# Kernel optimization log

Hardware: AMD Instinct MI355X
Metric: run time of the kernel (lower is better)

## Reference

```python
import jax, jax.numpy as jnp
import numpy as np
from jax import lax

B, N, S, P, FIN, FFUT, H, NB, TOPK = 4, 1437, 56, 28, 10, 6, 64, 2, 5


def layer_norm(x, g, b, eps=1e-5):
    m = x.mean(-1, keepdims=True)
    v = ((x - m) ** 2).mean(-1, keepdims=True)
    return (x - m) * lax.rsqrt(v + eps) * g + b


def conv1d_same(x, w, pl, pr):
    # x: [BNF, 1, S], w: [1, 1, k]; torch Conv1d is cross-correlation == XLA conv
    return lax.conv_general_dilated(x, w, (1,), [(pl, pr)], dimension_numbers=('NCH', 'OIH', 'NCH'))


def gelu(x):
    return jax.nn.gelu(x, approximate=False)


def mixer_block(x, adj, wk, mk, lcg, lcb, ltg, ltb, lfg, lfb, lsg, lsb, tw, tb, fw, fb, sw, sb):
    Bx, Nx, Sx, Fx = x.shape
    # conv branch (pre-norm)
    xn = layer_norm(x, lcg, lcb)
    xc = xn.transpose(0, 1, 3, 2).reshape(Bx * Nx * Fx, 1, Sx)
    weekly = conv1d_same(xc, wk, 3, 3).reshape(Bx, Nx, Fx, Sx).transpose(0, 1, 3, 2)
    monthly = conv1d_same(xc, mk, 13, 14).reshape(Bx, Nx, Fx, Sx).transpose(0, 1, 3, 2)
    x = x + weekly + monthly
    # temporal MLP over S
    xn = layer_norm(x, ltg, ltb)
    xt = gelu(jnp.einsum('bnfs,os->bnfo', xn.transpose(0, 1, 3, 2), tw) + tb)
    x = x + xt.transpose(0, 1, 3, 2)
    # feature MLP over Feat
    xn = layer_norm(x, lfg, lfb)
    x = x + gelu(jnp.einsum('bnsf,of->bnso', xn, fw) + fb)
    # spatial propagation via dense bmm with adj
    xn = layer_norm(x, lsg, lsb)
    xp = jnp.einsum('bnsf,of->bnso', xn, sw).reshape(Bx, Nx, Sx * Fx)
    xs = jnp.einsum('bmn,bnd->bmd', adj, xp).reshape(Bx, Nx, Sx, Fx) + sb
    return x + xs


def reference(x, x_future, adj, fp_w, fp_b, in_ln_g, in_ln_b, q_w, q_b, k_w, k_b,
              node_emb, graph_alpha, blk_weekly, blk_monthly,
              blk_lnc_g, blk_lnc_b, blk_lnt_g, blk_lnt_b, blk_lnf_g, blk_lnf_b,
              blk_lns_g, blk_lns_b, blk_temp_w, blk_temp_b, blk_feat_w, blk_feat_b,
              blk_spat_w, blk_spat_b, futr_w, futr_b, head_w, head_b):
    Bx, Nx, Sx, _ = x.shape
    h = jnp.einsum('bnsf,hf->bnsh', x, fp_w) + fp_b
    h = layer_norm(h, in_ln_g, in_ln_b)
    emb = node_emb / jnp.maximum(jnp.linalg.norm(node_emb, axis=-1, keepdims=True), 1e-12)
    h = h + emb[None, :, None, :]
    # recency-weighted context
    decay = jnp.exp(-jnp.arange(Sx, 0, -1, dtype=jnp.float32) / 14.0)
    rw = decay / decay.sum()
    ctx = (h * rw[None, None, :, None]).sum(2)  # [B,N,H]
    Q = ctx @ q_w.T + q_b
    K = ctx @ k_w.T + k_b
    da = jnp.einsum('bnh,bmh->bnm', Q, K) / jnp.sqrt(jnp.float32(Q.shape[-1]))
    da = jax.nn.relu(jnp.clip(da, -10.0, 10.0))
    _, ti = lax.top_k(da, TOPK)
    mask = jax.vmap(jax.vmap(lambda row, idx: row.at[idx].set(1.0)))(
        jnp.zeros((Bx, Nx, Nx), da.dtype), ti)
    dyn = jax.nn.softmax(jnp.where(mask > 0, da, -jnp.inf), axis=2)
    dyn = jnp.nan_to_num(dyn)
    alpha = jax.nn.sigmoid(graph_alpha)  # shape (1,), broadcasts
    comb = alpha * adj[None, :, :] + (1.0 - alpha) * dyn
    comb = comb / jnp.maximum(jnp.abs(comb).sum(axis=2, keepdims=True), 1e-12)
    for i in range(NB):
        h = mixer_block(h, comb, blk_weekly[i], blk_monthly[i],
                        blk_lnc_g[i], blk_lnc_b[i], blk_lnt_g[i], blk_lnt_b[i],
                        blk_lnf_g[i], blk_lnf_b[i], blk_lns_g[i], blk_lns_b[i],
                        blk_temp_w[i], blk_temp_b[i], blk_feat_w[i], blk_feat_b[i],
                        blk_spat_w[i], blk_spat_b[i])
    hist = h.reshape(Bx, Nx, -1)
    fut = (jnp.einsum('bnpf,hf->bnph', x_future, futr_w) + futr_b).reshape(Bx, Nx, -1)
    feats = jnp.concatenate([hist, fut], axis=2)
    return feats @ head_w.T + head_b


def setup_inputs() -> dict:
    key = jax.random.key(0)
    ks = jax.random.split(key, 16)
    rn = lambda k, shp, s=1.0: jax.random.normal(k, shp, dtype=jnp.float32) * s
    return {
        'x': rn(ks[0], (B, N, S, FIN)),
        'x_future': rn(ks[1], (B, N, P, FFUT)),
        'adj': jax.random.uniform(ks[2], (N, N), dtype=jnp.float32),
        'fp_w': rn(ks[3], (H, FIN), 0.1), 'fp_b': jnp.zeros((H,), jnp.float32),
        'in_ln_g': jnp.ones((H,), jnp.float32), 'in_ln_b': jnp.zeros((H,), jnp.float32),
        'q_w': rn(ks[4], (H, H), 0.1), 'q_b': jnp.zeros((H,), jnp.float32),
        'k_w': rn(ks[5], (H, H), 0.1), 'k_b': jnp.zeros((H,), jnp.float32),
        'node_emb': rn(ks[6], (N, H), 0.02),
        'graph_alpha': jnp.full((1,), 2.2, jnp.float32),
        'blk_weekly': rn(ks[7], (NB, 1, 1, 7), 0.1),
        'blk_monthly': rn(ks[8], (NB, 1, 1, 28), 0.1),
        'blk_lnc_g': jnp.ones((NB, H), jnp.float32), 'blk_lnc_b': jnp.zeros((NB, H), jnp.float32),
        'blk_lnt_g': jnp.ones((NB, H), jnp.float32), 'blk_lnt_b': jnp.zeros((NB, H), jnp.float32),
        'blk_lnf_g': jnp.ones((NB, H), jnp.float32), 'blk_lnf_b': jnp.zeros((NB, H), jnp.float32),
        'blk_lns_g': jnp.ones((NB, H), jnp.float32), 'blk_lns_b': jnp.zeros((NB, H), jnp.float32),
        'blk_temp_w': rn(ks[9], (NB, S, S), 0.1), 'blk_temp_b': jnp.zeros((NB, S), jnp.float32),
        'blk_feat_w': rn(ks[10], (NB, H, H), 0.1), 'blk_feat_b': jnp.zeros((NB, H), jnp.float32),
        'blk_spat_w': rn(ks[11], (NB, H, H), 0.1), 'blk_spat_b': jnp.zeros((NB, H), jnp.float32),
        'futr_w': rn(ks[12], (H, FFUT), 0.1), 'futr_b': jnp.zeros((H,), jnp.float32),
        'head_w': rn(ks[13], (P, S * H + P * H), 0.02), 'head_b': jnp.zeros((P,), jnp.float32),
    }
```

## Files before the change

### kernel.cpp

```cpp
#include <hip/hip_runtime.h>
#include <hip/hip_bf16.h>
#include <math.h>

#define BB 4
#define NN 1437
#define SS 56
#define PP 28
#define FIN 10
#define FFUT 6
#define HH 64
#define NBLK 2
#define TOPK 5
#define DD (SS*HH)
#define FD (PP*HH)
#define TOT (DD+FD)
#define MP 1536
#define KP 1472
#define KC8 (KP/8)
#define NT (KP/32)
#define WIMG_SZ 16384

typedef __attribute__((ext_vector_type(8))) __bf16 bf16x8;
typedef __attribute__((ext_vector_type(4))) float  f32x4;
typedef unsigned long long u64;


__device__ __forceinline__ float gelu_fast(float x){
    float x2 = x*x;
    float u  = __builtin_fmaf(0.044715f*x2, x, x);
    float e  = __builtin_amdgcn_exp2f(2.3022077f*u);
    float r  = __builtin_amdgcn_rcpf(e+1.f);
    return x - x*r;
}
template<int C>
__device__ __forceinline__ float dppadd(float v){
    int x = __builtin_amdgcn_mov_dpp(__float_as_int(v), C, 0xF, 0xF, true);
    return v + __int_as_float(x);
}
__device__ __forceinline__ float row16_sum(float v){
    v = dppadd<0xB1>(v);
    v = dppadd<0x4E>(v);
    v = dppadd<0x141>(v);
    v = dppadd<0x140>(v);
    return v;
}
__device__ __forceinline__ float wave_sum64(float v){
    v = row16_sum(v);
    v += __shfl_xor(v,16,64);
    v += __shfl_xor(v,32,64);
    return v;
}
__device__ __forceinline__ void async_load16(const void* g, void* l){
    __builtin_amdgcn_global_load_lds(
        (const __attribute__((address_space(1))) void*)g,
        (__attribute__((address_space(3))) void*)l, 16, 0, 0);
}
__device__ __forceinline__ unsigned short f2bf(float x){
    unsigned int u = __float_as_uint(x);
    unsigned int r = (u + 0x7fffu + ((u>>16)&1u)) >> 16;
    return (unsigned short)r;
}
__device__ __forceinline__ unsigned int cvtpk_bf16(float lo, float hi){
    unsigned int r;
    asm("v_cvt_pk_bf16_f32 %0, %1, %2" : "=v"(r) : "v"(lo), "v"(hi));
    return r;
}
__device__ __forceinline__ float bf2f(unsigned short u){
    return __uint_as_float(((unsigned int)u)<<16);
}
__device__ __forceinline__ unsigned char f2fp8(float x){
    return (unsigned char)(__builtin_amdgcn_cvt_pk_fp8_f32(x, 0.f, 0, false) & 0xFF);
}
__device__ __forceinline__ unsigned int pack4fp8(float a, float b, float c, float d){
    int lo = __builtin_amdgcn_cvt_pk_fp8_f32(a, b, 0, false);
    return (unsigned int)__builtin_amdgcn_cvt_pk_fp8_f32(c, d, lo, true);
}
__device__ __forceinline__ u64 umax64(u64 a, u64 b){return a>b?a:b;}
__device__ __forceinline__ u64 umin64(u64 a, u64 b){return a<b?a:b;}

#define INS5(a0,a1,a2,a3,a4,x) do{ u64 t_=(x); \
    u64 n0_=umax64(a0,t_), t1_=umin64(a0,t_); \
    u64 n1_=umax64(a1,t1_), t2_=umin64(a1,t1_); \
    u64 n2_=umax64(a2,t2_), t3_=umin64(a2,t2_); \
    u64 n3_=umax64(a3,t3_), t4_=umin64(a3,t3_); \
    u64 n4_=umax64(a4,t4_); \
    a0=n0_;a1=n1_;a2=n2_;a3=n3_;a4=n4_; }while(0)

#define MERGE5(a0,a1,a2,a3,a4,b0,b1,b2,b3,b4) do{ \
    u64 o0_=umax64(a0,(b0)); \
    u64 o1_=umax64(umax64((b1),umin64(a0,(b0))),a1); \
    u64 o2_=umax64(umax64((b2),umin64(a0,(b1))),umax64(umin64(a1,(b0)),a2)); \
    u64 o3_=umax64(umax64((b3),umin64(a0,(b2))),umax64(umin64(a1,(b1)),umax64(umin64(a2,(b0)),a3))); \
    u64 o4_=umax64(umax64((b4),umin64(a0,(b3))),umax64(umax64(umin64(a1,(b2)),umin64(a2,(b1))),umax64(umin64(a3,(b0)),a4))); \
    a0=o0_;a1=o1_;a2=o2_;a3=o3_;a4=o4_; }while(0)

__global__ __launch_bounds__(256) void k_front(
    const float* __restrict__ x, const float* __restrict__ fpw, const float* __restrict__ fpb,
    const float* __restrict__ lng, const float* __restrict__ lnb,
    const float* __restrict__ nemb,
    const float* __restrict__ qw, const float* __restrict__ qb,
    const float* __restrict__ kw, const float* __restrict__ kb,
    float* __restrict__ h,
    unsigned short* __restrict__ qpack, unsigned short* __restrict__ kpack)
{
    int bn = blockIdx.x; int n = bn % NN;
    int tid=threadIdx.x; int lane=tid&63; int wv=tid>>6;
    __shared__ float xin[SS*FIN];
    __shared__ float wlds[HH*FIN];
    __shared__ float rw[SS];
    __shared__ float rsum;
    __shared__ float red[4][HH];
    __shared__ float ctxs[HH];
    for (int i=tid;i<SS*FIN;i+=256) xin[i]=x[(size_t)bn*SS*FIN+i];
    for (int i=tid;i<HH*FIN;i+=256) wlds[i]=fpw[i];
    if (tid<SS) rw[tid]=expf(-(float)(SS-tid)/14.0f);
    __syncthreads();
    if (tid==0){ float s=0.f; for(int i=0;i<SS;++i) s+=rw[i]; rsum=s; }
    __syncthreads();
    float inv_rs = 1.0f/rsum;
    float ev = nemb[(size_t)n*HH+lane];
    float ss = wave_sum64(ev*ev);
    float el = ev / fmaxf(sqrtf(ss), 1e-12f);
    float gg=lng[lane], bv=lnb[lane], fb0=fpb[lane];
    int paddr = (lane&15)*4 + (lane>>4);
    float cacc=0.f;
    for (int s=wv;s<SS;s+=4){
        float v=fb0;
        #pragma unroll
        for (int c=0;c<FIN;++c) v += xin[s*FIN+c]*wlds[lane*FIN+c];
        float m = wave_sum64(v)*(1.f/HH);
        float d = v-m;
        float va = wave_sum64(d*d)*(1.f/HH);
        float hn = d*rsqrtf(va+1e-5f)*gg + bv + el;
        h[((size_t)bn*SS+s)*HH + paddr]=hn;
        cacc += hn * rw[s]*inv_rs;
    }
    red[wv][lane]=cacc;
    __syncthreads();
    if (wv==0) ctxs[lane]=red[0][lane]+red[1][lane]+red[2][lane]+red[3][lane];
    __syncthreads();
    if (wv==0){
        const float4* qr = reinterpret_cast<const float4*>(qw + (size_t)lane*HH);
        const float4* kr = reinterpret_cast<const float4*>(kw + (size_t)lane*HH);
        float q=qb[lane], k=kb[lane];
        #pragma unroll 4
        for (int t=0;t<16;++t){
            float4 qv=qr[t], kv=kr[t];
            float c0=ctxs[4*t], c1=ctxs[4*t+1], c2=ctxs[4*t+2], c3=ctxs[4*t+3];
            q += qv.x*c0+qv.y*c1+qv.z*c2+qv.w*c3;
            k += kv.x*c0+kv.y*c1+kv.z*c2+kv.w*c3;
        }
        int b = bn/NN, m = bn%NN;
        size_t off = (size_t)b*8*MP*8 + (size_t)(lane>>3)*MP*8 + (size_t)m*8 + (lane&7);
        qpack[off]=f2bf(q); kpack[off]=f2bf(k);
    }
}

__global__ __launch_bounds__(256) void k_adjsum(
    const float* __restrict__ adj, float* __restrict__ adjsum)
{
    int m = blockIdx.x*4 + (threadIdx.x>>6);
    int lane = threadIdx.x & 63;
    if (m >= NN) return;
    const float* row = adj + (size_t)m*NN;
    float s=0.f;
    for (int n=lane;n<NN;n+=64) s += row[n];
    s = wave_sum64(s);
    if (lane==0) adjsum[m]=s;
}

__global__ __launch_bounds__(256) void k_qkt_top5(
    const unsigned short* __restrict__ qp, const unsigned short* __restrict__ kp,
    const float* __restrict__ adjsum, const float* __restrict__ galpha,
    int* __restrict__ meta_idx, float* __restrict__ meta_p, float* __restrict__ meta_inv)
{
    int m0 = blockIdx.x*32; int b = blockIdx.y;
    int tid=threadIdx.x, lane=tid&63, w=tid>>6;
    int g=lane>>4, c15=lane&15;
    int wr=w>>1, wc=w&1;
    __shared__ u64 mls[64][5];

    const unsigned short* qb2 = qp + (size_t)b*8*MP*8;
    const unsigned short* kb2 = kp + (size_t)b*8*MP*8;
    bf16x8 af0 = *(const bf16x8*)(qb2 + ((size_t)(0*4+g)*MP + m0+wr*16+c15)*8);
    bf16x8 af1 = *(const bf16x8*)(qb2 + ((size_t)(1*4+g)*MP + m0+wr*16+c15)*8);

    u64 A0=0,A1=0,A2=0,A3=0,A4=0;
    u64 B0=0,B1=0,B2=0,B3=0,B4=0;
    u64 C0=0,C1=0,C2=0,C3=0,C4=0;
    u64 D0=0,D1=0,D2=0,D3=0,D4=0;

    for (int t=0;t<12;++t){
        int n0 = t*128;
        f32x4 acc[4];
        #pragma unroll
        for (int j=0;j<4;++j) acc[j]=(f32x4){0.f,0.f,0.f,0.f};
        #pragma unroll
        for (int j=0;j<4;++j){
            bf16x8 b0 = *(const bf16x8*)(kb2 + ((size_t)(0*4+g)*MP + n0+wc*64+j*16+c15)*8);
            bf16x8 b1 = *(const bf16x8*)(kb2 + ((size_t)(1*4+g)*MP + n0+wc*64+j*16+c15)*8);
            acc[j]=__builtin_amdgcn_mfma_f32_16x16x32_bf16(af0,b0,acc[j],0,0,0);
            acc[j]=__builtin_amdgcn_mfma_f32_16x16x32_bf16(af1,b1,acc[j],0,0,0);
        }
        #pragma unroll
        for (int j=0;j<4;++j){
            int n = n0 + wc*64 + j*16 + c15;
            bool ok = (n < NN);
            unsigned int lowk = 0xFFFFFFFFu - (unsigned)n;
            #define MKKEY(Q) ({ \
                float v_ = acc[j][Q]*0.125f; \
                v_ = fminf(fmaxf(v_,0.f),10.f); \
                ok ? (((u64)__float_as_uint(v_)<<32)|(u64)lowk) : 0ULL; })
            { u64 k_=MKKEY(0); INS5(A0,A1,A2,A3,A4,k_); }
            { u64 k_=MKKEY(1); INS5(B0,B1,B2,B3,B4,k_); }
            { u64 k_=MKKEY(2); INS5(C0,C1,C2,C3,C4,k_); }
            { u64 k_=MKKEY(3); INS5(D0,D1,D2,D3,D4,k_); }
            #undef MKKEY
        }
    }
    #pragma unroll
    for (int off=1; off<16; off<<=1){
        u64 t0,t1,t2,t3,t4;
        t0=__shfl_xor(A0,off,64); t1=__shfl_xor(A1,off,64); t2=__shfl_xor(A2,off,64); t3=__shfl_xor(A3,off,64); t4=__shfl_xor(A4,off,64);
        MERGE5(A0,A1,A2,A3,A4,t0,t1,t2,t3,t4);
        t0=__shfl_xor(B0,off,64); t1=__shfl_xor(B1,off,64); t2=__shfl_xor(B2,off,64); t3=__shfl_xor(B3,off,64); t4=__shfl_xor(B4,off,64);
        MERGE5(B0,B1,B2,B3,B4,t0,t1,t2,t3,t4);
        t0=__shfl_xor(C0,off,64); t1=__shfl_xor(C1,off,64); t2=__shfl_xor(C2,off,64); t3=__shfl_xor(C3,off,64); t4=__shfl_xor(C4,off,64);
        MERGE5(C0,C1,C2,C3,C4,t0,t1,t2,t3,t4);
        t0=__shfl_xor(D0,off,64); t1=__shfl_xor(D1,off,64); t2=__shfl_xor(D2,off,64); t3=__shfl_xor(D3,off,64); t4=__shfl_xor(D4,off,64);
        MERGE5(D0,D1,D2,D3,D4,t0,t1,t2,t3,t4);
    }
    if (c15==0){
        int rb = wr*16 + g*4;
        mls[(rb+0)*2+wc][0]=A0; mls[(rb+0)*2+wc][1]=A1; mls[(rb+0)*2+wc][2]=A2; mls[(rb+0)*2+wc][3]=A3; mls[(rb+0)*2+wc][4]=A4;
        mls[(rb+1)*2+wc][0]=B0; mls[(rb+1)*2+wc][1]=B1; mls[(rb+1)*2+wc][2]=B2; mls[(rb+1)*2+wc][3]=B3; mls[(rb+1)*2+wc][4]=B4;
        mls[(rb+2)*2+wc][0]=C0; mls[(rb+2)*2+wc][1]=C1; mls[(rb+2)*2+wc][2]=C2; mls[(rb+2)*2+wc][3]=C3; mls[(rb+2)*2+wc][4]=C4;
        mls[(rb+3)*2+wc][0]=D0; mls[(rb+3)*2+wc][1]=D1; mls[(rb+3)*2+wc][2]=D2; mls[(rb+3)*2+wc][3]=D3; mls[(rb+3)*2+wc][4]=D4;
    }
    __syncthreads();
    if (tid < 32){
        int m = m0 + tid;
        if (m < NN){
            u64 u0=mls[tid*2][0],u1=mls[tid*2][1],u2=mls[tid*2][2],u3=mls[tid*2][3],u4=mls[tid*2][4];
            MERGE5(u0,u1,u2,u3,u4, mls[tid*2+1][0],mls[tid*2+1][1],mls[tid*2+1][2],mls[tid*2+1][3],mls[tid*2+1][4]);
            float s0=__uint_as_float((unsigned)(u0>>32)), s1=__uint_as_float((unsigned)(u1>>32)),
                  s2=__uint_as_float((unsigned)(u2>>32)), s3=__uint_as_float((unsigned)(u3>>32)),
                  s4=__uint_as_float((unsigned)(u4>>32));
            int i0=(int)(0xFFFFFFFFu-(unsigned)u0), i1=(int)(0xFFFFFFFFu-(unsigned)u1),
                i2=(int)(0xFFFFFFFFu-(unsigned)u2), i3=(int)(0xFFFFFFFFu-(unsigned)u3),
                i4=(int)(0xFFFFFFFFu-(unsigned)u4);
            float e0=1.f, e1=expf(s1-s0), e2=expf(s2-s0), e3=expf(s3-s0), e4=expf(s4-s0);
            float den=e0+e1+e2+e3+e4;
            float alpha=1.f/(1.f+expf(-galpha[0]));
            float oma=(1.f-alpha)/den;
            size_t base = ((size_t)b*NN + m)*5;
            meta_idx[base+0]=i0; meta_idx[base+1]=i1; meta_idx[base+2]=i2; meta_idx[base+3]=i3; meta_idx[base+4]=i4;
            meta_p[base+0]=oma*e0; meta_p[base+1]=oma*e1; meta_p[base+2]=oma*e2; meta_p[base+3]=oma*e3; meta_p[base+4]=oma*e4;
            meta_inv[(size_t)b*NN+m] = 1.f/fmaxf(alpha*adjsum[m] + (1.f-alpha), 1e-12f);
        }
    }
}

__global__ __launch_bounds__(256) void k_blend(
    const float* __restrict__ adj, const float* __restrict__ galpha,
    const int* __restrict__ meta_idx, const float* __restrict__ meta_p,
    unsigned char* __restrict__ comb8)
{
    int bid = blockIdx.x;
    int xx = bid & 7, ii = bid >> 3;
    int lin = (xx < 4) ? xx*719 + ii : 2876 + (xx-4)*718 + ii;
    int b = lin / NN, m = lin - b*NN;
    int tid=threadIdx.x;
    size_t base = ((size_t)b*NN + m)*5;
    int i0=meta_idx[base+0], i1=meta_idx[base+1], i2=meta_idx[base+2],
        i3=meta_idx[base+3], i4=meta_idx[base+4];
    float p0=meta_p[base+0], p1=meta_p[base+1], p2=meta_p[base+2],
          p3=meta_p[base+3], p4=meta_p[base+4];
    float alpha=1.f/(1.f+expf(-galpha[0]));
    const float* arow = adj + (size_t)m*NN;
    unsigned char* dst = comb8 + (size_t)b*KC8*(size_t)MP*8;
    for (int n4=tid; n4<KP/4; n4+=256){
        float v[4];
        #pragma unroll
        for (int k=0;k<4;++k){
            int n = n4*4+k;
            float vv = 0.f;
            if (n<NN){
                vv = alpha*arow[n];
                vv += (n==i0)?p0:0.f;
                vv += (n==i1)?p1:0.f;
                vv += (n==i2)?p2:0.f;
                vv += (n==i3)?p3:0.f;
                vv += (n==i4)?p4:0.f;
            }
            v[k]=vv;
        }
        int kc = n4>>1, half = n4&1;
        *reinterpret_cast<unsigned int*>(dst + ((size_t)kc*MP + m)*8 + half*4) =
            pack4fp8(v[0],v[1],v[2],v[3]);
    }
}

__global__ __launch_bounds__(256) void k_prepw(
    const float* __restrict__ wk, const float* __restrict__ mk,
    const float* __restrict__ tw, const float* __restrict__ fw,
    const float* __restrict__ sw, unsigned short* __restrict__ wimg)
{
    int i = blockIdx.x; int tid = threadIdx.x;
    const float* wki = wk + i*7;
    const float* mki = mk + i*28;
    const float* twi = tw + i*SS*SS;
    const float* fwi = fw + i*HH*HH;
    const float* swi = sw + i*HH*HH;
    unsigned short* o = wimg + (size_t)i*WIMG_SZ;
    for (int e=tid; e<4096; e+=256){
        int r = e>>6, k = e&63;
        int swz = ((k*2) ^ ((r&7)<<4)) >> 1;
        float mv = 0.f;
        if (r<SS && k<SS){
            int a = k-r+3;  if (a>=0 && a<7)  mv += wki[a];
            int b2= k-r+13; if (b2>=0 && b2<28) mv += mki[b2];
        }
        o[r*64 + swz] = f2bf(mv);
        float tv = (r<SS && k<SS) ? twi[r*SS+k] : 0.f;
        o[4096 + r*64 + swz] = f2bf(tv);
        int pk = (k>>3)*512 + r*8 + (k&7);
        o[8192  + pk] = f2bf(fwi[r*HH+k]);
        o[12288 + pk] = f2bf(swi[r*HH+k]);
    }
}

__global__ __launch_bounds__(256) void k_prep_head(
    const float* __restrict__ hw, __hip_bfloat16* __restrict__ hw16)
{
    int i = blockIdx.x*256 + threadIdx.x;
    int r = i / TOT, k = i - r*TOT;
    float v = (r<PP) ? hw[(size_t)r*TOT + k] : 0.f;
    hw16[i] = __float2bfloat16(v);
}

__global__ __launch_bounds__(256) void k_fut(
    const float* __restrict__ xf, const float* __restrict__ fw,
    const float* __restrict__ fbias, __hip_bfloat16* __restrict__ feats)
{
    int bn=blockIdx.x, tid=threadIdx.x;
    __shared__ float fwl[HH*FFUT];
    __shared__ float fbl[HH];
    __shared__ float xfl[PP*FFUT];
    for (int i=tid;i<HH*FFUT;i+=256) fwl[i]=fw[i];
    if (tid<HH) fbl[tid]=fbias[tid];
    for (int i=tid;i<PP*FFUT;i+=256) xfl[i]=xf[(size_t)bn*PP*FFUT+i];
    __syncthreads();
    __hip_bfloat16* dst = feats + (size_t)bn*TOT + DD;
    for (int q=tid;q<FD;q+=256){
        int pp=q>>6, hh2=q&63;
        float v=fbl[hh2];
        #pragma unroll
        for (int c2=0;c2<FFUT;++c2) v += xfl[pp*FFUT+c2]*fwl[hh2*FFUT+c2];
        dst[q]=__float2bfloat16(v);
    }
}

__global__ __launch_bounds__(256) void k_mixer2(
    float* __restrict__ h, unsigned char* __restrict__ xpg8,
    const unsigned short* __restrict__ spat_in,
    const unsigned short* __restrict__ wimg,
    const float* __restrict__ lncg, const float* __restrict__ lncb,
    const float* __restrict__ lntg, const float* __restrict__ lntb,
    const float* __restrict__ lnfg, const float* __restrict__ lnfb,
    const float* __restrict__ lnsg, const float* __restrict__ lnsb,
    const float* __restrict__ tb, const float* __restrict__ fb)
{
    int bid = blockIdx.x;
    int xx = bid & 7, ii = bid >> 3;
    int bn = (xx < 4) ? xx*719 + ii : 2876 + (xx-4)*718 + ii;
    int tid=threadIdx.x, lane=tid&63, w=tid>>6;
    int g=lane>>4, c=lane&15;
    __shared__ unsigned short wbuf[2][4096];
    __shared__ unsigned short xsA[4096];
    __shared__ unsigned short xsB[4096];
    __shared__ float prm[640];

    const char* wsrc=(const char*)wimg;
#define LOADW(SLOTB, BUFP) do{ \
    async_load16(wsrc+(size_t)(SLOTB)+((size_t)tid)*16,       (char*)(BUFP)+(w*64)*16); \
    async_load16(wsrc+(size_t)(SLOTB)+((size_t)(256+tid))*16, (char*)(BUFP)+((256+w*64))*16); } while(0)

    LOADW(0,    wbuf[0]);
    LOADW(8192, wbuf[1]);
    if (tid<64){
        prm[tid]      =lncg[tid]; prm[64+tid] =lncb[tid];
        prm[128+tid]  =lntg[tid]; prm[192+tid]=lntb[tid];
        prm[256+tid]  =lnfg[tid]; prm[320+tid]=lnfb[tid];
        prm[384+tid]  =lnsg[tid]; prm[448+tid]=lnsb[tid];
        prm[512+tid]  =(tid<SS)?tb[tid]:0.f;
        prm[576+tid]  =fb[tid];
    }
    float xl[4][4];
    float* hb = h + (size_t)bn*DD;
    int srow = 16*w + 4*g;
    #pragma unroll
    for (int q=0;q<4;++q){
        int s=srow+q;
        if (s<SS){
            const float4 v4 = *reinterpret_cast<const float4*>(hb + s*HH + c*4);
            float a0=v4.x, a1=v4.y, a2=v4.z, a3=v4.w;
            if (spat_in){
                ushort4 sv = *reinterpret_cast<const ushort4*>(spat_in + (size_t)bn*TOT + s*HH + c*4);
                a0 += bf2f(sv.x); a1 += bf2f(sv.y); a2 += bf2f(sv.z); a3 += bf2f(sv.w);
            }
            xl[q][0]=a0; xl[q][1]=a1; xl[q][2]=a2; xl[q][3]=a3;
        } else {
            xl[q][0]=0.f; xl[q][1]=0.f; xl[q][2]=0.f; xl[q][3]=0.f;
        }
    }
    __syncthreads();

    float xn[4][4];
    f32x4 acc[4];

#define LNSTAGE(GOFF,BOFF) do{ \
    _Pragma("unroll") \
    for (int q=0;q<4;++q){ \
        float sv = xl[q][0]+xl[q][1]+xl[q][2]+xl[q][3]; \
        float s2 = xl[q][0]*xl[q][0]+xl[q][1]*xl[q][1]+xl[q][2]*xl[q][2]+xl[q][3]*xl[q][3]; \
        sv = row16_sum(sv); \
        s2 = row16_sum(s2); \
        float mn = sv*(1.f/64.f); \
        float var = s2*(1.f/64.f)-mn*mn; \
        float rstd = rsqrtf(var+1e-5f); \
        bool ok = (srow+q)<SS; \
        _Pragma("unroll") \
        for (int tj=0;tj<4;++tj){ \
            float v=(xl[q][tj]-mn)*rstd*prm[(GOFF)+tj*16+c]+prm[(BOFF)+tj*16+c]; \
            xn[q][tj]= ok ? v : 0.f; \
        } \
    } }while(0)

#define WRITE_XNP(XS) do{ \
    _Pragma("unroll") \
    for (int qp=0;qp<2;++qp){ \
        int s0=srow+2*qp; \
        _Pragma("unroll") \
        for (int tj=0;tj<4;++tj){ \
            unsigned int pv = cvtpk_bf16(xn[2*qp][tj], xn[2*qp+1][tj]); \
            *(unsigned int*)((char*)(XS) + ((s0>>3)*1024 + (tj*16+c)*16 + (s0&7)*2)) = pv; \
        } \
    } }while(0)

#define WRITE_XNR(XS) do{ \
    _Pragma("unroll") \
    for (int q=0;q<4;++q){ int s=srow+q; \
        _Pragma("unroll") \
        for (int tj=0;tj<4;++tj){ \
            *(unsigned short*)((char*)(XS) + s*128 + (((tj*16+c)*2) ^ ((s&7)<<4))) = f2bf(xn[q][tj]); \
        } \
    } }while(0)

#define MM(APTR,BPTR) do{ \
    _Pragma("unroll") \
    for (int tj=0;tj<4;++tj) acc[tj]=(f32x4){0.f,0.f,0.f,0.f}; \
    _Pragma("unroll") \
    for (int kc=0;kc<2;++kc){ \
        int arow=16*w+c; \
        bf16x8 af=*(const bf16x8*)((const char*)(APTR)+arow*128+((kc*64+g*16)^((arow&7)<<4))); \
        _Pragma("unroll") \
        for (int tj=0;tj<4;++tj){ \
            bf16x8 bf2=*(const bf16x8*)((const char*)(BPTR)+(kc*4+g)*1024+(tj*16+c)*16); \
            acc[tj]=__builtin_amdgcn_mfma_f32_16x16x32_bf16(af,bf2,acc[tj],0,0,0); \
        } \
    } }while(0)

    LNSTAGE(0,64); WRITE_XNP(xsA);
    __syncthreads();
    MM(&wbuf[0][0], xsA);
    #pragma unroll
    for (int q=0;q<4;++q)
        #pragma unroll
        for (int tj=0;tj<4;++tj) xl[q][tj]+=acc[tj][q];
    LNSTAGE(128,192); WRITE_XNP(xsB);
    __syncthreads();
    LOADW(16384, wbuf[0]);
    MM(&wbuf[1][0], xsB);
    #pragma unroll
    for (int q=0;q<4;++q){
        float tbv=prm[512+srow+q];
        #pragma unroll
        for (int tj=0;tj<4;++tj) xl[q][tj]+=gelu_fast(acc[tj][q]+tbv);
    }
    LNSTAGE(256,320); WRITE_XNR(xsA);
    __syncthreads();
    LOADW(24576, wbuf[1]);
    MM(xsA, &wbuf[0][0]);
    #pragma unroll
    for (int q=0;q<4;++q)
        #pragma unroll
        for (int tj=0;tj<4;++tj) xl[q][tj]+=gelu_fast(acc[tj][q]+prm[576+tj*16+c]);
    LNSTAGE(384,448); WRITE_XNR(xsB);
    __syncthreads();
    MM(xsB, &wbuf[1][0]);
    int b_=bn/NN, n_=bn%NN;
    unsigned char* xpo = xpg8 + ((size_t)b_*KC8 + (size_t)(n_>>3))*(size_t)DD*8 + (n_&7);
    #pragma unroll
    for (int q=0;q<4;++q){
        int s=srow+q;
        if (s<SS){
            float4 hv; hv.x=xl[q][0]; hv.y=xl[q][1]; hv.z=xl[q][2]; hv.w=xl[q][3];
            *reinterpret_cast<float4*>(hb + s*HH + c*4) = hv;
            #pragma unroll
            for (int tj=0;tj<4;++tj){
                int d = s*HH + tj*16 + c;
                xpo[(size_t)d*8] = f2fp8(acc[tj][q]);
            }
        }
    }
#undef LNSTAGE
#undef WRITE_XNP
#undef WRITE_XNR
#undef MM
#undef LOADW
}

__global__ __launch_bounds__(256,8) void k_bmm_mfma(
    const unsigned char* __restrict__ comb8,
    const unsigned char* __restrict__ xpg8,
    const float* __restrict__ sb,
    const float* __restrict__ h,
    const float* __restrict__ meta_inv,
    unsigned short* __restrict__ spat_out,
    __hip_bfloat16* __restrict__ feats_out)
{
    __shared__ unsigned char As8[3][2048];
    __shared__ unsigned char Bs8[3][4096];
    __shared__ float sinv[64];

    int bid = blockIdx.x;
    int wg = (bid & 7)*336 + (bid >> 3);
    int bm = wg % 24; int tmp2 = wg / 24; int bd = tmp2 % 28; int b = tmp2 / 28;
    int tid=threadIdx.x, lane=tid&63, w=tid>>6;
    int g=lane>>4, c=lane&15;
    int wr=w>>1, wc=w&1;
    int m0=bm*64, d0=bd*128;

    const unsigned char* cbK = comb8 + (size_t)b*KC8*(size_t)MP*8;
    const unsigned char* xb  = xpg8  + (size_t)b*KC8*(size_t)DD*8;

    int l32 = lane & 31;
    const unsigned char* srcA = cbK + ((size_t)w*MP + m0 + l32*2)*8;
    const size_t ASTEP = (size_t)4*MP*8;
    int klB = tid>>6, dpair = tid&63;
    const unsigned char* srcB = xb + ((size_t)klB*DD + d0 + dpair*2)*8;
    const size_t BSTEP = (size_t)4*DD*8;

    if (tid < 64){
        int m = m0 + tid;
        sinv[tid] = (m < NN) ? meta_inv[(size_t)b*NN + m] : 0.f;
    }

    f32x4 acc[2][4];
    #pragma unroll
    for (int i=0;i<2;++i)
        #pragma unroll
        for (int j=0;j<4;++j) acc[i][j]=(f32x4){0.f,0.f,0.f,0.f};

    int aoff[2], boff[4];
    #pragma unroll
    for (int i=0;i<2;++i) aoff[i] = g*512 + (32*wr + 16*i + c)*8;
    #pragma unroll
    for (int j=0;j<4;++j) boff[j] = g*1024 + (64*wc + 16*j + c)*8;

#define STAGE(BUF,T) do { \
    if (lane < 32) async_load16(srcA + (size_t)(T)*ASTEP, (char*)As8[BUF] + w*512 + l32*16); \
    async_load16(srcB + (size_t)(T)*BSTEP, (char*)Bs8[BUF] + tid*16); } while(0)

    STAGE(0,0); STAGE(1,1);
    asm volatile("s_waitcnt vmcnt(2) lgkmcnt(0)" ::: "memory");
    __builtin_amdgcn_s_barrier();

    int cur=0;
    for (int t=0;t<NT;++t){
        if (t+2<NT){
            int nb = cur+2; if (nb>=3) nb-=3;
            STAGE(nb, t+2);
        }
        const char* Ab=(const char*)As8[cur];
        const char* Bb=(const char*)Bs8[cur];
        u64 af[2], bfv[4];
        #pragma unroll
        for (int i=0;i<2;++i) af[i]=*(const u64*)(Ab + aoff[i]);
        #pragma unroll
        for (int j=0;j<4;++j) bfv[j]=*(const u64*)(Bb + boff[j]);
        #pragma unroll
        for (int i=0;i<2;++i)
            #pragma unroll
            for (int j=0;j<4;++j)
                acc[i][j]=__builtin_amdgcn_mfma_f32_16x16x32_fp8_fp8((long)af[i],(long)bfv[j],acc[i][j],0,0,0);
        if (t+2<NT) asm volatile("s_waitcnt vmcnt(2)" ::: "memory");
        else        asm volatile("s_waitcnt vmcnt(0)" ::: "memory");
        __builtin_amdgcn_s_barrier();
        ++cur; if (cur>=3) cur=0;
    }
#undef STAGE

    int row_b = m0 + 32*wr + g*4;
    int s2 = 2*bd + wc;
    float sb0=sb[c], sb1=sb[16+c], sb2=sb[32+c], sb3=sb[48+c];
    #pragma unroll
    for (int i=0;i<2;++i){
        #pragma unroll
        for (int q=0;q<4;++q){
            int m = row_b + 16*i + q;
            if (m < NN){
                float inv = sinv[32*wr + g*4 + 16*i + q];
                if (spat_out){
                    ushort4 pv;
                    pv.x = f2bf(inv*acc[i][0][q] + sb0);
                    pv.y = f2bf(inv*acc[i][1][q] + sb1);
                    pv.z = f2bf(inv*acc[i][2][q] + sb2);
                    pv.w = f2bf(inv*acc[i][3][q] + sb3);
                    *reinterpret_cast<ushort4*>(spat_out + ((size_t)b*NN+m)*TOT + s2*HH + c*4) = pv;
                } else {
                    const float* hp = h + ((size_t)b*NN+m)*DD + s2*HH + c*4;
                    float4 hv = *reinterpret_cast<const float4*>(hp);
                    float nv0 = hv.x + inv*acc[i][0][q] + sb0;
                    float nv1 = hv.y + inv*acc[i][1][q] + sb1;
                    float nv2 = hv.z + inv*acc[i][2][q] + sb2;
                    float nv3 = hv.w + inv*acc[i][3][q] + sb3;
                    size_t fr = ((size_t)b*NN+m)*TOT + (size_t)bd*128 + wc*64;
                    feats_out[fr + c]      = __float2bfloat16(nv0);
                    feats_out[fr + 16 + c] = __float2bfloat16(nv1);
                    feats_out[fr + 32 + c] = __float2bfloat16(nv2);
                    feats_out[fr + 48 + c] = __float2bfloat16(nv3);
                }
            }
        }
    }
}

__global__ __launch_bounds__(256) void k_head_mfma(
    const __hip_bfloat16* __restrict__ feats, const __hip_bfloat16* __restrict__ hw16,
    const float* __restrict__ hb, float* __restrict__ out)
{
    int tid=threadIdx.x, lane=tid&63, w=tid>>6;
    int g=lane>>4, c=lane&15;
    int m0=blockIdx.x*32;
    int rt=w>>1, pt=w&1;
    int arow = m0 + rt*16 + c;
    if (arow > BB*NN-1) arow = BB*NN-1;
    const char* abase = (const char*)feats + (size_t)arow*TOT*2 + g*16;
    const char* bbase = (const char*)hw16 + (size_t)(pt*16+c)*TOT*2 + g*16;
    f32x4 acc=(f32x4){0.f,0.f,0.f,0.f};
    #pragma unroll 4
    for (int kc=0;kc<TOT/32;++kc){
        bf16x8 af =*(const bf16x8*)(abase + (size_t)kc*64);
        bf16x8 bf2=*(const bf16x8*)(bbase + (size_t)kc*64);
        acc=__builtin_amdgcn_mfma_f32_16x16x32_bf16(af,bf2,acc,0,0,0);
    }
    int col = pt*16 + c;
    #pragma unroll
    for (int q=0;q<4;++q){
        int row = m0 + rt*16 + g*4 + q;
        if (row < BB*NN && col < PP)
            out[(size_t)row*PP + col] = acc[q] + hb[col];
    }
}

extern "C" void kernel_launch(void* const* d_in, const int* in_sizes, int n_in,
                              void* d_out, int out_size, void* d_ws, size_t ws_size,
                              hipStream_t stream)
{
    const float* x      = (const float*)d_in[0];
    const float* xfut   = (const float*)d_in[1];
    const float* adj    = (const float*)d_in[2];
    const float* fp_w   = (const float*)d_in[3];
    const float* fp_b   = (const float*)d_in[4];
    const float* inlng  = (const float*)d_in[5];
    const float* inlnb  = (const float*)d_in[6];
    const float* q_w    = (const float*)d_in[7];
    const float* q_b    = (const float*)d_in[8];
    const float* k_w    = (const float*)d_in[9];
    const float* k_b    = (const float*)d_in[10];
    const float* nemb   = (const float*)d_in[11];
    const float* galpha = (const float*)d_in[12];
    const float* wk     = (const float*)d_in[13];
    const float* mk     = (const float*)d_in[14];
    const float* lncg   = (const float*)d_in[15];
    const float* lncb   = (const float*)d_in[16];
    const float* lntg   = (const float*)d_in[17];
    const float* lntb   = (const float*)d_in[18];
    const float* lnfg   = (const float*)d_in[19];
    const float* lnfb   = (const float*)d_in[20];
    const float* lnsg   = (const float*)d_in[21];
    const float* lnsb   = (const float*)d_in[22];
    const float* tw     = (const float*)d_in[23];
    const float* tb     = (const float*)d_in[24];
    const float* fw     = (const float*)d_in[25];
    const float* fb     = (const float*)d_in[26];
    const float* sw     = (const float*)d_in[27];
    const float* sb     = (const float*)d_in[28];
    const float* futw   = (const float*)d_in[29];
    const float* futb   = (const float*)d_in[30];
    const float* hw     = (const float*)d_in[31];
    const float* hb     = (const float*)d_in[32];
    (void)in_sizes; (void)n_in; (void)out_size; (void)ws_size;
    float* out = (float*)d_out;
    float* ws = (float*)d_ws;
    const size_t HSZ = (size_t)BB*NN*SS*HH;

    float* h = ws;
    unsigned char* comb8 = (unsigned char*)(h + HSZ);
    unsigned char* xpg8  = comb8 + (size_t)BB*KC8*(size_t)MP*8;
    unsigned short* wimg  = (unsigned short*)(xpg8 + (size_t)BB*KC8*(size_t)DD*8);
    unsigned short* qpack = wimg + (size_t)NBLK*WIMG_SZ;
    unsigned short* kpack = qpack + (size_t)BB*8*MP*8;
    __hip_bfloat16* feats16 = (__hip_bfloat16*)(kpack + (size_t)BB*8*MP*8);
    __hip_bfloat16* hw16    = feats16 + (size_t)BB*NN*TOT;
    float* adjsum   = (float*)(hw16 + (size_t)32*TOT);
    int*   meta_idx = (int*)(adjsum + NN);
    float* meta_p   = (float*)(meta_idx + (size_t)BB*NN*5);
    float* meta_inv = meta_p + (size_t)BB*NN*5;

    k_prepw<<<NBLK,256,0,stream>>>(wk, mk, tw, fw, sw, wimg);
    k_prep_head<<<(32*TOT)/256,256,0,stream>>>(hw, hw16);
    k_adjsum<<<(NN+3)/4,256,0,stream>>>(adj, adjsum);
    k_fut<<<BB*NN,256,0,stream>>>(xfut, futw, futb, feats16);
    k_front<<<BB*NN,256,0,stream>>>(x, fp_w, fp_b, inlng, inlnb, nemb,
                                    q_w,q_b,k_w,k_b, h, qpack, kpack);
    dim3 gq5(MP/32, BB);
    k_qkt_top5<<<gq5,256,0,stream>>>(qpack, kpack, adjsum, galpha,
                                     meta_idx, meta_p, meta_inv);
    k_blend<<<BB*NN,256,0,stream>>>(adj, galpha, meta_idx, meta_p, comb8);
    for (int b2=0;b2<BB;++b2)
        hipMemsetAsync(xpg8 + ((size_t)b2*KC8+179)*(size_t)DD*8, 0,
                       (size_t)5*DD*8, stream);
    k_mixer2<<<BB*NN,256,0,stream>>>(h, xpg8, (const unsigned short*)nullptr,
        wimg, lncg,lncb, lntg,lntb, lnfg,lnfb, lnsg,lnsb, tb, fb);
    k_bmm_mfma<<<2688,256,0,stream>>>(comb8, xpg8, sb, h, meta_inv,
        (unsigned short*)feats16, (__hip_bfloat16*)nullptr);
    k_mixer2<<<BB*NN,256,0,stream>>>(h, xpg8, (const unsigned short*)feats16,
        wimg + WIMG_SZ, lncg+HH,lncb+HH, lntg+HH,lntb+HH, lnfg+HH,lnfb+HH, lnsg+HH,lnsb+HH,
        tb+SS, fb+HH);
    k_bmm_mfma<<<2688,256,0,stream>>>(comb8, xpg8, sb+HH, h, meta_inv,
        (unsigned short*)nullptr, feats16);
    k_head_mfma<<<(BB*NN+31)/32,256,0,stream>>>(feats16, hw16, hb, out);
}
```

Baseline: 444.9 us.

## Process two nodes per mixer block, split q/k across waves, multi-accumulate head

The mixer kernel now launches 512-thread blocks that each handle two (b,n) nodes. The node pair shares one weight-image load into LDS, so per-node weight traffic and block count are halved, at the cost of more LDS per block and a new bid-to-node mapping. The front kernel computes the q and k projections on two separate waves instead of one. The head GEMM uses four independent MFMA accumulators to break the dependency chain on a single accumulator.

```diff
diff --git a/kernel.cpp b/kernel.cpp
--- a/kernel.cpp
+++ b/kernel.cpp
@@ -139,20 +139,20 @@
     __syncthreads();
     if (wv==0) ctxs[lane]=red[0][lane]+red[1][lane]+red[2][lane]+red[3][lane];
     __syncthreads();
-    if (wv==0){
-        const float4* qr = reinterpret_cast<const float4*>(qw + (size_t)lane*HH);
-        const float4* kr = reinterpret_cast<const float4*>(kw + (size_t)lane*HH);
-        float q=qb[lane], k=kb[lane];
+    if (wv<2){
+        const float* wmat = (wv==0)? qw : kw;
+        const float* bvec = (wv==0)? qb : kb;
+        unsigned short* dstp = (wv==0)? qpack : kpack;
+        const float4* wr_ = reinterpret_cast<const float4*>(wmat + (size_t)lane*HH);
+        float acc = bvec[lane];
         #pragma unroll 4
         for (int t=0;t<16;++t){
-            float4 qv=qr[t], kv=kr[t];
-            float c0=ctxs[4*t], c1=ctxs[4*t+1], c2=ctxs[4*t+2], c3=ctxs[4*t+3];
-            q += qv.x*c0+qv.y*c1+qv.z*c2+qv.w*c3;
-            k += kv.x*c0+kv.y*c1+kv.z*c2+kv.w*c3;
+            float4 wv4=wr_[t];
+            acc += wv4.x*ctxs[4*t] + wv4.y*ctxs[4*t+1] + wv4.z*ctxs[4*t+2] + wv4.w*ctxs[4*t+3];
         }
         int b = bn/NN, m = bn%NN;
         size_t off = (size_t)b*8*MP*8 + (size_t)(lane>>3)*MP*8 + (size_t)m*8 + (lane&7);
-        qpack[off]=f2bf(q); kpack[off]=f2bf(k);
+        dstp[off]=f2bf(acc);
     }
 }
 
@@ -361,7 +361,7 @@
     }
 }
 
-__global__ __launch_bounds__(256) void k_mixer2(
+__global__ __launch_bounds__(512) void k_mixer2(
     float* __restrict__ h, unsigned char* __restrict__ xpg8,
     const unsigned short* __restrict__ spat_in,
     const unsigned short* __restrict__ wimg,
@@ -373,18 +373,18 @@
 {
     int bid = blockIdx.x;
     int xx = bid & 7, ii = bid >> 3;
-    int bn = (xx < 4) ? xx*719 + ii : 2876 + (xx-4)*718 + ii;
+    int lin = (xx < 2) ? xx*360 + ii : 720 + (xx-2)*359 + ii;
     int tid=threadIdx.x, lane=tid&63, w=tid>>6;
+    int half = w>>2, wloc = w&3;
+    int bn = 2*lin + half;
     int g=lane>>4, c=lane&15;
     __shared__ unsigned short wbuf[2][4096];
-    __shared__ unsigned short xsA[4096];
-    __shared__ unsigned short xsB[4096];
+    __shared__ unsigned short xs[2][2][4096];
     __shared__ float prm[640];
 
     const char* wsrc=(const char*)wimg;
-#define LOADW(SLOTB, BUFP) do{ \
-    async_load16(wsrc+(size_t)(SLOTB)+((size_t)tid)*16,       (char*)(BUFP)+(w*64)*16); \
-    async_load16(wsrc+(size_t)(SLOTB)+((size_t)(256+tid))*16, (char*)(BUFP)+((256+w*64))*16); } while(0)
+#define LOADW(SLOTB, BUFP) \
+    async_load16(wsrc+(size_t)(SLOTB)+((size_t)tid)*16, (char*)(BUFP)+tid*16)
 
     LOADW(0,    wbuf[0]);
     LOADW(8192, wbuf[1]);
@@ -398,7 +398,7 @@
     }
     float xl[4][4];
     float* hb = h + (size_t)bn*DD;
-    int srow = 16*w + 4*g;
+    int srow = 16*wloc + 4*g;
     #pragma unroll
     for (int q=0;q<4;++q){
         int s=srow+q;
@@ -462,7 +462,7 @@
     for (int tj=0;tj<4;++tj) acc[tj]=(f32x4){0.f,0.f,0.f,0.f}; \
     _Pragma("unroll") \
     for (int kc=0;kc<2;++kc){ \
-        int arow=16*w+c; \
+        int arow=16*wloc+c; \
         bf16x8 af=*(const bf16x8*)((const char*)(APTR)+arow*128+((kc*64+g*16)^((arow&7)<<4))); \
         _Pragma("unroll") \
         for (int tj=0;tj<4;++tj){ \
@@ -471,34 +471,34 @@
         } \
     } }while(0)
 
-    LNSTAGE(0,64); WRITE_XNP(xsA);
-    __syncthreads();
-    MM(&wbuf[0][0], xsA);
+    LNSTAGE(0,64); WRITE_XNP(xs[half][0]);
+    __syncthreads();
+    MM(&wbuf[0][0], xs[half][0]);
     #pragma unroll
     for (int q=0;q<4;++q)
         #pragma unroll
         for (int tj=0;tj<4;++tj) xl[q][tj]+=acc[tj][q];
-    LNSTAGE(128,192); WRITE_XNP(xsB);
+    LNSTAGE(128,192); WRITE_XNP(xs[half][1]);
     __syncthreads();
     LOADW(16384, wbuf[0]);
-    MM(&wbuf[1][0], xsB);
+    MM(&wbuf[1][0], xs[half][1]);
     #pragma unroll
     for (int q=0;q<4;++q){
         float tbv=prm[512+srow+q];
         #pragma unroll
         for (int tj=0;tj<4;++tj) xl[q][tj]+=gelu_fast(acc[tj][q]+tbv);
     }
-    LNSTAGE(256,320); WRITE_XNR(xsA);
+    LNSTAGE(256,320); WRITE_XNR(xs[half][0]);
     __syncthreads();
     LOADW(24576, wbuf[1]);
-    MM(xsA, &wbuf[0][0]);
+    MM(xs[half][0], &wbuf[0][0]);
     #pragma unroll
     for (int q=0;q<4;++q)
         #pragma unroll
         for (int tj=0;tj<4;++tj) xl[q][tj]+=gelu_fast(acc[tj][q]+prm[576+tj*16+c]);
-    LNSTAGE(384,448); WRITE_XNR(xsB);
-    __syncthreads();
-    MM(xsB, &wbuf[1][0]);
+    LNSTAGE(384,448); WRITE_XNR(xs[half][1]);
+    __syncthreads();
+    MM(xs[half][1], &wbuf[1][0]);
     int b_=bn/NN, n_=bn%NN;
     unsigned char* xpo = xpg8 + ((size_t)b_*KC8 + (size_t)(n_>>3))*(size_t)DD*8 + (n_&7);
     #pragma unroll
@@ -649,13 +649,22 @@
     if (arow > BB*NN-1) arow = BB*NN-1;
     const char* abase = (const char*)feats + (size_t)arow*TOT*2 + g*16;
     const char* bbase = (const char*)hw16 + (size_t)(pt*16+c)*TOT*2 + g*16;
-    f32x4 acc=(f32x4){0.f,0.f,0.f,0.f};
-    #pragma unroll 4
-    for (int kc=0;kc<TOT/32;++kc){
-        bf16x8 af =*(const bf16x8*)(abase + (size_t)kc*64);
-        bf16x8 bf2=*(const bf16x8*)(bbase + (size_t)kc*64);
-        acc=__builtin_amdgcn_mfma_f32_16x16x32_bf16(af,bf2,acc,0,0,0);
-    }
+    f32x4 a0=(f32x4){0.f,0.f,0.f,0.f}, a1=a0, a2=a0, a3=a0;
+    for (int kc=0;kc<TOT/32;kc+=4){
+        bf16x8 af0 =*(const bf16x8*)(abase + (size_t)kc*64);
+        bf16x8 bf0 =*(const bf16x8*)(bbase + (size_t)kc*64);
+        bf16x8 af1 =*(const bf16x8*)(abase + (size_t)(kc+1)*64);
+        bf16x8 bf1 =*(const bf16x8*)(bbase + (size_t)(kc+1)*64);
+        bf16x8 af2 =*(const bf16x8*)(abase + (size_t)(kc+2)*64);
+        bf16x8 bf2 =*(const bf16x8*)(bbase + (size_t)(kc+2)*64);
+        bf16x8 af3 =*(const bf16x8*)(abase + (size_t)(kc+3)*64);
+        bf16x8 bf3 =*(const bf16x8*)(bbase + (size_t)(kc+3)*64);
+        a0=__builtin_amdgcn_mfma_f32_16x16x32_bf16(af0,bf0,a0,0,0,0);
+        a1=__builtin_amdgcn_mfma_f32_16x16x32_bf16(af1,bf1,a1,0,0,0);
+        a2=__builtin_amdgcn_mfma_f32_16x16x32_bf16(af2,bf2,a2,0,0,0);
+        a3=__builtin_amdgcn_mfma_f32_16x16x32_bf16(af3,bf3,a3,0,0,0);
+    }
+    f32x4 acc = (a0+a1)+(a2+a3);
     int col = pt*16 + c;
     #pragma unroll
     for (int q=0;q<4;++q){
@@ -733,11 +742,11 @@
     for (int b2=0;b2<BB;++b2)
         hipMemsetAsync(xpg8 + ((size_t)b2*KC8+179)*(size_t)DD*8, 0,
                        (size_t)5*DD*8, stream);
-    k_mixer2<<<BB*NN,256,0,stream>>>(h, xpg8, (const unsigned short*)nullptr,
+    k_mixer2<<<2874,512,0,stream>>>(h, xpg8, (const unsigned short*)nullptr,
         wimg, lncg,lncb, lntg,lntb, lnfg,lnfb, lnsg,lnsb, tb, fb);
     k_bmm_mfma<<<2688,256,0,stream>>>(comb8, xpg8, sb, h, meta_inv,
         (unsigned short*)feats16, (__hip_bfloat16*)nullptr);
-    k_mixer2<<<BB*NN,256,0,stream>>>(h, xpg8, (const unsigned short*)feats16,
+    k_mixer2<<<2874,512,0,stream>>>(h, xpg8, (const unsigned short*)feats16,
         wimg + WIMG_SZ, lncg+HH,lncb+HH, lntg+HH,lntb+HH, lnfg+HH,lnfb+HH, lnsg+HH,lnsb+HH,
         tb+SS, fb+HH);
     k_bmm_mfma<<<2688,256,0,stream>>>(comb8, xpg8, sb+HH, h, meta_inv,
```

New measurement: 454.3 us. +2.1%, slower.

## Split head GEMM along K across four blocks with separate reduction kernel

Applied to the files above, without the earlier changes.

The head projection GEMM now splits its K dimension into four slices via a second grid dimension, so the launch has four times as many blocks to fill the GPU. Each block writes partial sums to a workspace buffer, and a new elementwise kernel adds the four partials and the bias. The inner loop also uses two independent MFMA accumulators to hide MFMA latency. The cost is an extra kernel launch and extra global traffic for the partial buffer.

```diff
diff --git a/kernel.cpp b/kernel.cpp
--- a/kernel.cpp
+++ b/kernel.cpp
@@ -639,29 +639,47 @@
 
 __global__ __launch_bounds__(256) void k_head_mfma(
     const __hip_bfloat16* __restrict__ feats, const __hip_bfloat16* __restrict__ hw16,
-    const float* __restrict__ hb, float* __restrict__ out)
+    float* __restrict__ hpart)
 {
     int tid=threadIdx.x, lane=tid&63, w=tid>>6;
     int g=lane>>4, c=lane&15;
     int m0=blockIdx.x*32;
+    int kq=blockIdx.y;
     int rt=w>>1, pt=w&1;
     int arow = m0 + rt*16 + c;
     if (arow > BB*NN-1) arow = BB*NN-1;
     const char* abase = (const char*)feats + (size_t)arow*TOT*2 + g*16;
     const char* bbase = (const char*)hw16 + (size_t)(pt*16+c)*TOT*2 + g*16;
-    f32x4 acc=(f32x4){0.f,0.f,0.f,0.f};
-    #pragma unroll 4
-    for (int kc=0;kc<TOT/32;++kc){
-        bf16x8 af =*(const bf16x8*)(abase + (size_t)kc*64);
-        bf16x8 bf2=*(const bf16x8*)(bbase + (size_t)kc*64);
-        acc=__builtin_amdgcn_mfma_f32_16x16x32_bf16(af,bf2,acc,0,0,0);
-    }
+    f32x4 a0=(f32x4){0.f,0.f,0.f,0.f}, a1=a0;
+    int kbeg = kq*42, kend = kbeg+42;
+    for (int kc=kbeg;kc<kend;kc+=2){
+        bf16x8 af0 =*(const bf16x8*)(abase + (size_t)kc*64);
+        bf16x8 bf0 =*(const bf16x8*)(bbase + (size_t)kc*64);
+        bf16x8 af1 =*(const bf16x8*)(abase + (size_t)(kc+1)*64);
+        bf16x8 bf1 =*(const bf16x8*)(bbase + (size_t)(kc+1)*64);
+        a0=__builtin_amdgcn_mfma_f32_16x16x32_bf16(af0,bf0,a0,0,0,0);
+        a1=__builtin_amdgcn_mfma_f32_16x16x32_bf16(af1,bf1,a1,0,0,0);
+    }
+    f32x4 acc = a0+a1;
     int col = pt*16 + c;
     #pragma unroll
     for (int q=0;q<4;++q){
         int row = m0 + rt*16 + g*4 + q;
         if (row < BB*NN && col < PP)
-            out[(size_t)row*PP + col] = acc[q] + hb[col];
+            hpart[((size_t)kq*BB*NN + row)*PP + col] = acc[q];
+    }
+}
+
+__global__ __launch_bounds__(256) void k_head_red(
+    const float* __restrict__ hpart, const float* __restrict__ hb,
+    float* __restrict__ out)
+{
+    int idx = blockIdx.x*256 + threadIdx.x;
+    const int NTOT = BB*NN*PP;
+    if (idx < NTOT){
+        float v = hpart[idx] + hpart[(size_t)NTOT + idx]
+                + hpart[(size_t)2*NTOT + idx] + hpart[(size_t)3*NTOT + idx];
+        out[idx] = v + hb[idx % PP];
     }
 }
 
@@ -719,6 +737,7 @@
     int*   meta_idx = (int*)(adjsum + NN);
     float* meta_p   = (float*)(meta_idx + (size_t)BB*NN*5);
     float* meta_inv = meta_p + (size_t)BB*NN*5;
+    float* hpart    = meta_inv + (size_t)BB*NN;
 
     k_prepw<<<NBLK,256,0,stream>>>(wk, mk, tw, fw, sw, wimg);
     k_prep_head<<<(32*TOT)/256,256,0,stream>>>(hw, hw16);
@@ -742,5 +761,7 @@
         tb+SS, fb+HH);
     k_bmm_mfma<<<2688,256,0,stream>>>(comb8, xpg8, sb+HH, h, meta_inv,
         (unsigned short*)nullptr, feats16);
-    k_head_mfma<<<(BB*NN+31)/32,256,0,stream>>>(feats16, hw16, hb, out);
-}
+    dim3 ghead((BB*NN+31)/32, 4);
+    k_head_mfma<<<ghead,256,0,stream>>>(feats16, hw16, hpart);
+    k_head_red<<<(BB*NN*PP+255)/256,256,0,stream>>>(hpart, hb, out);
+}
```

After: 431.4 us. 1.03x faster.
